# Performance work log

Measured on AMD Instinct MI355X. Metric: run time of the kernel, lower is better.

Reference implementation:

```python
import jax, jax.numpy as jnp
import numpy as np

# ---- module hyperparameters (from init_kwargs) ----
K_CURV = 1.0      # Lorentz curvature k
MAX_NORM = 1000.0 # rescale_to_max cap on space-norm (assumed)
KSIZE = 5
STRIDE = 2
PAD = 2
IN_CH = 257       # includes time dim -> 256 space channels
OUT_CH = 257
LIN_FEATS = (IN_CH - 1) * KSIZE + 1  # 1281
EPS = 1e-8


def _add_time(space):
    # time = sqrt(k + ||space||^2), concat on last axis
    time = jnp.sqrt(K_CURV + jnp.sum(space * space, axis=-1, keepdims=True))
    return jnp.concatenate([time, space], axis=-1)


def _rescale_to_max(x):
    # clamp space-norm to MAX_NORM, then recompute valid time component
    space = x[..., 1:]
    norm = jnp.sqrt(jnp.sum(space * space, axis=-1, keepdims=True))
    scale = jnp.minimum(1.0, MAX_NORM / jnp.maximum(norm, EPS))
    return _add_time(space * scale)


def setup_inputs() -> dict:
    key = jax.random.key(0)
    kx, kw, kb = jax.random.split(key, 3)
    x = jax.random.normal(kx, (16, 8192, IN_CH), dtype=jnp.float32)
    W = jax.random.normal(kw, (OUT_CH, LIN_FEATS), dtype=jnp.float32) * 0.02
    b = jax.random.normal(kb, (OUT_CH,), dtype=jnp.float32) * 0.01
    return {"x": x, "W": W, "b": b}


def reference(x, W, b):
    B, L, C = x.shape
    # pad length dim with zeros (time channel of padded frames is clamped in
    # torch, but the time channel is discarded before add_time, so only the
    # space channels matter)
    xp = jnp.pad(x, ((0, 0), (PAD, PAD), (0, 0)))
    space = xp[..., 1:]                                  # (B, Lp, C-1)
    Lp = L + 2 * PAD
    n_frames = (Lp - KSIZE) // STRIDE + 1
    # im2col gather: (n_frames, K) window indices
    idx = jnp.arange(n_frames)[:, None] * STRIDE + jnp.arange(KSIZE)[None, :]
    patches = space[:, idx, :]                           # (B, n, K, C-1)
    # torch reorders to kernel-major (k, c) layout before add_time
    ps = patches.reshape(B, n_frames, KSIZE * (C - 1))   # (B, n, K*(C-1))
    pk = _add_time(ps)                                   # (B, n, lin_feats)
    out = jnp.einsum('bnf,of->bno', pk, W) + b           # LorentzProjection
    out = _add_time(out[..., 1:])                        # manifold.projx
    out = _rescale_to_max(out)                           # rescale_after=True
    return out
```

## Files before the change

### kernel.cpp

```cpp
#include <hip/hip_runtime.h>
#include <hip/hip_bf16.h>
#include <cstdint>
#include <cstddef>

namespace {

constexpr int BATCH = 16;
constexpr int LEN   = 8192;
constexpr int CIN   = 257;
constexpr int CS    = 256;
constexpr int NF    = 4096;
constexpr int KG    = 1280;
constexpr int MT    = 128;
constexpr int NITER = 20;

constexpr size_t WT_BYTES = (size_t)CS * KG * 2;
constexpr size_t W0_OFF   = WT_BYTES;
constexpr size_t WS_NEED  = W0_OFF + (size_t)CS * 4;

typedef __attribute__((ext_vector_type(8))) short short8;
typedef __attribute__((ext_vector_type(8))) unsigned short ushort8v;
typedef __attribute__((ext_vector_type(4))) float f32x4;

__device__ __forceinline__ unsigned short f2bf_bits(float f) {
  union { __hip_bfloat16 h; unsigned short u; } cv;
  cv.h = __float2bfloat16(f);
  return cv.u;
}

__device__ __forceinline__ void async_cp16(const void* g, void* l) {
  __builtin_amdgcn_global_load_lds(
      (const __attribute__((address_space(1))) void*)g,
      (__attribute__((address_space(3))) void*)l,
      16, 0, 0);
}

}

__global__ void prep_w_kernel(const float* __restrict__ W,
                              __hip_bfloat16* __restrict__ wt,
                              float* __restrict__ w0) {
  int n = blockIdx.x;
  const float* wrow = W + (size_t)(n + 1) * 1281;
  for (int k = threadIdx.x; k < KG; k += blockDim.x)
    wt[(size_t)n * KG + k] = __float2bfloat16(wrow[1 + k]);
  if (threadIdx.x == 0) w0[n] = wrow[0];
}

__global__ __launch_bounds__(512, 2) void lorentz_fused_kernel(
    const float* __restrict__ x,
    const __hip_bfloat16* __restrict__ wt,
    const float* __restrict__ w0,
    const float* __restrict__ bvec,
    float* __restrict__ out) {
  __shared__ alignas(16) char A_lds[16384];
  __shared__ alignas(16) char B_lds[32768];
  __shared__ alignas(16) float time0_s[128];
  __shared__ alignas(16) float normsq_s[128];

  const int tid   = threadIdx.x;
  const int w     = tid >> 6;
  const int lane  = tid & 63;
  const int row16 = lane & 15;
  const int q     = lane >> 4;
  const int mh    = w >> 2;
  const int nq    = w & 3;
  const int lg    = lane >> 3;
  const int lc    = lane & 7;
  const int csw   = lc ^ lg;

  const int bx    = blockIdx.x;
  const int b     = bx >> 5;
  const int Mblk  = (bx & 31) * MT;

  const int m0 = w * 16 + lg;
  const int m1 = m0 + 8;
  const float* xb = x + (size_t)b * LEN * CIN;

  f32x4 acc[4][4];
#pragma unroll
  for (int i = 0; i < 4; ++i)
#pragma unroll
    for (int j = 0; j < 4; ++j) acc[i][j] = (f32x4){0.f, 0.f, 0.f, 0.f};

  float ssq0 = 0.f, ssq1 = 0.f;
  f32x4 a00, a01, a10, a11;

  auto loadA = [&](int it) {
    const int kk = it >> 2;
    const int c0 = (it & 3) << 6;
    const int coff = 1 + c0 + lc * 8;
    const int t0 = 2 * (Mblk + m0) + kk - 2;
    const int t1 = t0 + 16;
    a00 = (f32x4){0.f, 0.f, 0.f, 0.f};
    a01 = a00; a10 = a00; a11 = a00;
    if ((unsigned)t0 < (unsigned)LEN) {
      const float* g = xb + (size_t)t0 * CIN + coff;
      __builtin_memcpy(&a00, g, 16);
      __builtin_memcpy(&a01, g + 4, 16);
    }
    if ((unsigned)t1 < (unsigned)LEN) {
      const float* g = xb + (size_t)t1 * CIN + coff;
      __builtin_memcpy(&a10, g, 16);
      __builtin_memcpy(&a11, g + 4, 16);
    }
  };

  auto writeA = [&]() {
    ssq0 += a00[0]*a00[0] + a00[1]*a00[1] + a00[2]*a00[2] + a00[3]*a00[3]
          + a01[0]*a01[0] + a01[1]*a01[1] + a01[2]*a01[2] + a01[3]*a01[3];
    ssq1 += a10[0]*a10[0] + a10[1]*a10[1] + a10[2]*a10[2] + a10[3]*a10[3]
          + a11[0]*a11[0] + a11[1]*a11[1] + a11[2]*a11[2] + a11[3]*a11[3];
    ushort8v u0, u1;
#pragma unroll
    for (int i = 0; i < 4; ++i) {
      u0[i]     = f2bf_bits(a00[i]);
      u0[4 + i] = f2bf_bits(a01[i]);
      u1[i]     = f2bf_bits(a10[i]);
      u1[4 + i] = f2bf_bits(a11[i]);
    }
    *(ushort8v*)(A_lds + ((m0 * 8 + csw) << 4)) = u0;
    *(ushort8v*)(A_lds + ((m1 * 8 + csw) << 4)) = u1;
  };

  auto stageB = [&](int it) {
    const int k0 = it << 6;
#pragma unroll
    for (int j = 0; j < 4; ++j) {
      const int n = w * 32 + j * 8 + lg;
      async_cp16(wt + (size_t)n * KG + k0 + csw * 8, B_lds + (w * 4 + j) * 1024);
    }
  };

  auto compute = [&]() {
#pragma unroll
    for (int s = 0; s < 2; ++s) {
      const int p = (s * 4 + q) ^ lc;
      short8 bfr[4];
#pragma unroll
      for (int nt = 0; nt < 4; ++nt)
        bfr[nt] = *(const short8*)(B_lds + (((nq * 64 + nt * 16 + row16) * 8 + p) << 4));
#pragma unroll
      for (int mt = 0; mt < 4; ++mt) {
        short8 af = *(const short8*)(A_lds + (((mh * 64 + mt * 16 + row16) * 8 + p) << 4));
#pragma unroll
        for (int nt = 0; nt < 4; ++nt)
          acc[mt][nt] = __builtin_amdgcn_mfma_f32_16x16x32_bf16(
              af, bfr[nt], acc[mt][nt], 0, 0, 0);
      }
    }
  };

  loadA(0);
  for (int it = 0; it < NITER; ++it) {
    __syncthreads();
    writeA();
    stageB(it);
    if (it + 1 < NITER) loadA(it + 1);
    __syncthreads();
    compute();
  }

  __syncthreads();
  if (tid < 128) normsq_s[tid] = 0.0f;
  {
    float s0 = ssq0;
    s0 += __shfl_xor(s0, 1); s0 += __shfl_xor(s0, 2); s0 += __shfl_xor(s0, 4);
    float s1 = ssq1;
    s1 += __shfl_xor(s1, 1); s1 += __shfl_xor(s1, 2); s1 += __shfl_xor(s1, 4);
    if (lc == 0) {
      time0_s[m0] = sqrtf(1.0f + s0);
      time0_s[m1] = sqrtf(1.0f + s1);
    }
  }
  __syncthreads();

  float w0v[4], bv[4];
#pragma unroll
  for (int nt = 0; nt < 4; ++nt) {
    int n = nq * 64 + nt * 16 + row16;
    w0v[nt] = w0[n];
    bv[nt]  = bvec[1 + n];
  }

#pragma unroll
  for (int mt = 0; mt < 4; ++mt) {
    f32x4 t4 = *(const f32x4*)&time0_s[mh * 64 + mt * 16 + q * 4];
#pragma unroll
    for (int nt = 0; nt < 4; ++nt)
#pragma unroll
      for (int r = 0; r < 4; ++r)
        acc[mt][nt][r] = acc[mt][nt][r] + t4[r] * w0v[nt] + bv[nt];
#pragma unroll
    for (int r = 0; r < 4; ++r) {
      float ps = 0.f;
#pragma unroll
      for (int nt = 0; nt < 4; ++nt) ps += acc[mt][nt][r] * acc[mt][nt][r];
      ps += __shfl_xor(ps, 1);
      ps += __shfl_xor(ps, 2);
      ps += __shfl_xor(ps, 4);
      ps += __shfl_xor(ps, 8);
      if (row16 == 0) atomicAdd(&normsq_s[mh * 64 + mt * 16 + q * 4 + r], ps);
    }
  }
  __syncthreads();

#pragma unroll
  for (int mt = 0; mt < 4; ++mt) {
#pragma unroll
    for (int r = 0; r < 4; ++r) {
      int m = mh * 64 + mt * 16 + q * 4 + r;
      float nsq  = normsq_s[m];
      float norm = sqrtf(nsq);
      float scale = fminf(1.0f, 1000.0f / fmaxf(norm, 1e-8f));
      size_t ob = ((size_t)b * NF + Mblk + m) * 257;
#pragma unroll
      for (int nt = 0; nt < 4; ++nt) {
        int n = nq * 64 + nt * 16 + row16;
        out[ob + 1 + n] = acc[mt][nt][r] * scale;
      }
    }
  }
  if (tid < 128) {
    float nsq  = normsq_s[tid];
    float norm = sqrtf(nsq);
    float scale = fminf(1.0f, 1000.0f / fmaxf(norm, 1e-8f));
    size_t ob = ((size_t)b * NF + Mblk + tid) * 257;
    out[ob] = sqrtf(1.0f + scale * scale * nsq);
  }
}

__global__ void fallback_kernel(const float* __restrict__ x,
                                const float* __restrict__ W,
                                const float* __restrict__ bvec,
                                float* __restrict__ out) {
  int fid = blockIdx.x;
  int b = fid >> 12;
  int g = fid & (NF - 1);
  __shared__ float patch[1280];
  __shared__ float red[256];
  int tid = threadIdx.x;
  float ss = 0.f;
  for (int k = tid; k < 1280; k += 256) {
    int kk = k >> 8, c = k & 255;
    int t = 2 * g + kk - 2;
    float v = (t >= 0 && t < LEN) ? x[((size_t)b * LEN + t) * CIN + 1 + c] : 0.f;
    patch[k] = v;
    ss += v * v;
  }
  red[tid] = ss;
  __syncthreads();
  for (int off = 128; off > 0; off >>= 1) {
    if (tid < off) red[tid] += red[tid + off];
    __syncthreads();
  }
  float time0 = sqrtf(1.f + red[0]);
  __syncthreads();
  const float* wrow = W + (size_t)(tid + 1) * 1281;
  float acc = time0 * wrow[0] + bvec[tid + 1];
  for (int k = 0; k < 1280; ++k) acc += wrow[1 + k] * patch[k];
  red[tid] = acc * acc;
  __syncthreads();
  for (int off = 128; off > 0; off >>= 1) {
    if (tid < off) red[tid] += red[tid + off];
    __syncthreads();
  }
  float nsq = red[0];
  float norm = sqrtf(nsq);
  float scale = fminf(1.f, 1000.f / fmaxf(norm, 1e-8f));
  size_t ob = ((size_t)b * NF + g) * 257;
  out[ob + 1 + tid] = acc * scale;
  if (tid == 0) out[ob] = sqrtf(1.f + scale * scale * nsq);
}

extern "C" void kernel_launch(void* const* d_in, const int* in_sizes, int n_in,
                              void* d_out, int out_size, void* d_ws, size_t ws_size,
                              hipStream_t stream) {
  const float* x  = (const float*)d_in[0];
  const float* W  = (const float*)d_in[1];
  const float* bv = (const float*)d_in[2];
  float* out = (float*)d_out;

  if (ws_size >= WS_NEED) {
    char* ws = (char*)d_ws;
    __hip_bfloat16* wt = (__hip_bfloat16*)ws;
    float* w0          = (float*)(ws + W0_OFF);
    prep_w_kernel<<<256, 256, 0, stream>>>(W, wt, w0);
    lorentz_fused_kernel<<<BATCH * (NF / MT), 512, 0, stream>>>(x, wt, w0, bv, out);
  } else {
    fallback_kernel<<<BATCH * NF, 256, 0, stream>>>(x, W, bv, out);
  }
}
```

Before: 285.5 us.

## Drop LDS staging and feed MFMA fragments directly from global memory

```diff
diff --git a/kernel.cpp b/kernel.cpp
--- a/kernel.cpp
+++ b/kernel.cpp
@@ -19,20 +19,14 @@
 constexpr size_t WS_NEED  = W0_OFF + (size_t)CS * 4;
 
 typedef __attribute__((ext_vector_type(8))) short short8;
-typedef __attribute__((ext_vector_type(8))) unsigned short ushort8v;
 typedef __attribute__((ext_vector_type(4))) float f32x4;
+
+union bfpack { unsigned short u[8]; short8 s; };
 
 __device__ __forceinline__ unsigned short f2bf_bits(float f) {
   union { __hip_bfloat16 h; unsigned short u; } cv;
   cv.h = __float2bfloat16(f);
   return cv.u;
-}
-
-__device__ __forceinline__ void async_cp16(const void* g, void* l) {
-  __builtin_amdgcn_global_load_lds(
-      (const __attribute__((address_space(1))) void*)g,
-      (__attribute__((address_space(3))) void*)l,
-      16, 0, 0);
 }
 
 }
@@ -47,14 +41,12 @@
   if (threadIdx.x == 0) w0[n] = wrow[0];
 }
 
-__global__ __launch_bounds__(512, 2) void lorentz_fused_kernel(
+__global__ __launch_bounds__(512, 4) void lorentz_fused_kernel(
     const float* __restrict__ x,
     const __hip_bfloat16* __restrict__ wt,
     const float* __restrict__ w0,
     const float* __restrict__ bvec,
     float* __restrict__ out) {
-  __shared__ alignas(16) char A_lds[16384];
-  __shared__ alignas(16) char B_lds[32768];
   __shared__ alignas(16) float time0_s[128];
   __shared__ alignas(16) float normsq_s[128];
 
@@ -63,131 +55,113 @@
   const int lane  = tid & 63;
   const int row16 = lane & 15;
   const int q     = lane >> 4;
-  const int mh    = w >> 2;
-  const int nq    = w & 3;
-  const int lg    = lane >> 3;
-  const int lc    = lane & 7;
-  const int csw   = lc ^ lg;
+  const int wm    = w >> 1;
+  const int wn    = w & 1;
 
   const int bx    = blockIdx.x;
   const int b     = bx >> 5;
   const int Mblk  = (bx & 31) * MT;
 
-  const int m0 = w * 16 + lg;
-  const int m1 = m0 + 8;
   const float* xb = x + (size_t)b * LEN * CIN;
-
-  f32x4 acc[4][4];
-#pragma unroll
-  for (int i = 0; i < 4; ++i)
-#pragma unroll
-    for (int j = 0; j < 4; ++j) acc[i][j] = (f32x4){0.f, 0.f, 0.f, 0.f};
-
+  const int frame0 = Mblk + wm * 32 + row16;
+
+  f32x4 acc[2][8];
+#pragma unroll
+  for (int i = 0; i < 2; ++i)
+#pragma unroll
+    for (int j = 0; j < 8; ++j) acc[i][j] = (f32x4){0.f, 0.f, 0.f, 0.f};
+
+  f32x4 afA[2][4], afB[2][4];
   float ssq0 = 0.f, ssq1 = 0.f;
-  f32x4 a00, a01, a10, a11;
-
-  auto loadA = [&](int it) {
-    const int kk = it >> 2;
-    const int c0 = (it & 3) << 6;
-    const int coff = 1 + c0 + lc * 8;
-    const int t0 = 2 * (Mblk + m0) + kk - 2;
-    const int t1 = t0 + 16;
-    a00 = (f32x4){0.f, 0.f, 0.f, 0.f};
-    a01 = a00; a10 = a00; a11 = a00;
-    if ((unsigned)t0 < (unsigned)LEN) {
-      const float* g = xb + (size_t)t0 * CIN + coff;
-      __builtin_memcpy(&a00, g, 16);
-      __builtin_memcpy(&a01, g + 4, 16);
-    }
-    if ((unsigned)t1 < (unsigned)LEN) {
-      const float* g = xb + (size_t)t1 * CIN + coff;
-      __builtin_memcpy(&a10, g, 16);
-      __builtin_memcpy(&a11, g + 4, 16);
-    }
-  };
-
-  auto writeA = [&]() {
-    ssq0 += a00[0]*a00[0] + a00[1]*a00[1] + a00[2]*a00[2] + a00[3]*a00[3]
-          + a01[0]*a01[0] + a01[1]*a01[1] + a01[2]*a01[2] + a01[3]*a01[3];
-    ssq1 += a10[0]*a10[0] + a10[1]*a10[1] + a10[2]*a10[2] + a10[3]*a10[3]
-          + a11[0]*a11[0] + a11[1]*a11[1] + a11[2]*a11[2] + a11[3]*a11[3];
-    ushort8v u0, u1;
+
+  auto loadA = [&](int it, f32x4 (&af)[2][4]) {
+#pragma unroll
+    for (int mt = 0; mt < 2; ++mt) {
+      const int t = 2 * (frame0 + mt * 16) + (it >> 2) - 2;
+      af[mt][0] = (f32x4){0.f, 0.f, 0.f, 0.f};
+      af[mt][1] = af[mt][0];
+      af[mt][2] = af[mt][0];
+      af[mt][3] = af[mt][0];
+      if ((unsigned)t < (unsigned)LEN) {
+        const float* g = xb + (size_t)t * CIN + 1 + ((it & 3) << 6) + q * 8;
+        __builtin_memcpy(&af[mt][0], g, 16);
+        __builtin_memcpy(&af[mt][1], g + 4, 16);
+        __builtin_memcpy(&af[mt][2], g + 32, 16);
+        __builtin_memcpy(&af[mt][3], g + 36, 16);
+      }
+    }
+  };
+
+  auto cvt2 = [&](const f32x4& lo, const f32x4& hi) -> short8 {
+    bfpack p;
 #pragma unroll
     for (int i = 0; i < 4; ++i) {
-      u0[i]     = f2bf_bits(a00[i]);
-      u0[4 + i] = f2bf_bits(a01[i]);
-      u1[i]     = f2bf_bits(a10[i]);
-      u1[4 + i] = f2bf_bits(a11[i]);
-    }
-    *(ushort8v*)(A_lds + ((m0 * 8 + csw) << 4)) = u0;
-    *(ushort8v*)(A_lds + ((m1 * 8 + csw) << 4)) = u1;
-  };
-
-  auto stageB = [&](int it) {
-    const int k0 = it << 6;
-#pragma unroll
-    for (int j = 0; j < 4; ++j) {
-      const int n = w * 32 + j * 8 + lg;
-      async_cp16(wt + (size_t)n * KG + k0 + csw * 8, B_lds + (w * 4 + j) * 1024);
-    }
-  };
-
-  auto compute = [&]() {
-#pragma unroll
-    for (int s = 0; s < 2; ++s) {
-      const int p = (s * 4 + q) ^ lc;
-      short8 bfr[4];
-#pragma unroll
-      for (int nt = 0; nt < 4; ++nt)
-        bfr[nt] = *(const short8*)(B_lds + (((nq * 64 + nt * 16 + row16) * 8 + p) << 4));
-#pragma unroll
-      for (int mt = 0; mt < 4; ++mt) {
-        short8 af = *(const short8*)(A_lds + (((mh * 64 + mt * 16 + row16) * 8 + p) << 4));
-#pragma unroll
-        for (int nt = 0; nt < 4; ++nt)
-          acc[mt][nt] = __builtin_amdgcn_mfma_f32_16x16x32_bf16(
-              af, bfr[nt], acc[mt][nt], 0, 0, 0);
+      p.u[i]     = f2bf_bits(lo[i]);
+      p.u[4 + i] = f2bf_bits(hi[i]);
+    }
+    return p.s;
+  };
+
+  auto mfma_half = [&](int it, int s, f32x4 (&cur)[2][4]) {
+    const int ko = (it << 6) + s * 32 + q * 8;
+    short8 bb[8];
+#pragma unroll
+    for (int nt = 0; nt < 8; ++nt) {
+      const int n = wn * 128 + nt * 16 + row16;
+      bb[nt] = *(const short8*)(wt + (size_t)n * KG + ko);
+    }
+    short8 ab0 = cvt2(cur[0][s * 2], cur[0][s * 2 + 1]);
+    short8 ab1 = cvt2(cur[1][s * 2], cur[1][s * 2 + 1]);
+    if (wn == 0) {
+#pragma unroll
+      for (int i = 0; i < 4; ++i) {
+        ssq0 += cur[0][s*2][i] * cur[0][s*2][i] + cur[0][s*2+1][i] * cur[0][s*2+1][i];
+        ssq1 += cur[1][s*2][i] * cur[1][s*2][i] + cur[1][s*2+1][i] * cur[1][s*2+1][i];
       }
     }
-  };
-
-  loadA(0);
-  for (int it = 0; it < NITER; ++it) {
-    __syncthreads();
-    writeA();
-    stageB(it);
-    if (it + 1 < NITER) loadA(it + 1);
-    __syncthreads();
-    compute();
-  }
-
-  __syncthreads();
+#pragma unroll
+    for (int nt = 0; nt < 8; ++nt) {
+      acc[0][nt] = __builtin_amdgcn_mfma_f32_16x16x32_bf16(ab0, bb[nt], acc[0][nt], 0, 0, 0);
+      acc[1][nt] = __builtin_amdgcn_mfma_f32_16x16x32_bf16(ab1, bb[nt], acc[1][nt], 0, 0, 0);
+    }
+  };
+
+  auto body = [&](int it, f32x4 (&cur)[2][4], f32x4 (&nxt)[2][4]) {
+    if (it + 1 < NITER) loadA(it + 1, nxt);
+    mfma_half(it, 0, cur);
+    mfma_half(it, 1, cur);
+  };
+
+  loadA(0, afA);
+  for (int it = 0; it < NITER; it += 2) {
+    body(it,     afA, afB);
+    body(it + 1, afB, afA);
+  }
+
   if (tid < 128) normsq_s[tid] = 0.0f;
   {
-    float s0 = ssq0;
-    s0 += __shfl_xor(s0, 1); s0 += __shfl_xor(s0, 2); s0 += __shfl_xor(s0, 4);
-    float s1 = ssq1;
-    s1 += __shfl_xor(s1, 1); s1 += __shfl_xor(s1, 2); s1 += __shfl_xor(s1, 4);
-    if (lc == 0) {
-      time0_s[m0] = sqrtf(1.0f + s0);
-      time0_s[m1] = sqrtf(1.0f + s1);
-    }
-  }
-  __syncthreads();
-
-  float w0v[4], bv[4];
-#pragma unroll
-  for (int nt = 0; nt < 4; ++nt) {
-    int n = nq * 64 + nt * 16 + row16;
+    float s0 = ssq0; s0 += __shfl_xor(s0, 16); s0 += __shfl_xor(s0, 32);
+    float s1 = ssq1; s1 += __shfl_xor(s1, 16); s1 += __shfl_xor(s1, 32);
+    if (wn == 0 && q == 0) {
+      time0_s[wm * 32 + row16]      = sqrtf(1.0f + s0);
+      time0_s[wm * 32 + 16 + row16] = sqrtf(1.0f + s1);
+    }
+  }
+  __syncthreads();
+
+  float w0v[8], bv[8];
+#pragma unroll
+  for (int nt = 0; nt < 8; ++nt) {
+    int n = wn * 128 + nt * 16 + row16;
     w0v[nt] = w0[n];
     bv[nt]  = bvec[1 + n];
   }
 
 #pragma unroll
-  for (int mt = 0; mt < 4; ++mt) {
-    f32x4 t4 = *(const f32x4*)&time0_s[mh * 64 + mt * 16 + q * 4];
-#pragma unroll
-    for (int nt = 0; nt < 4; ++nt)
+  for (int mt = 0; mt < 2; ++mt) {
+    f32x4 t4 = *(const f32x4*)&time0_s[wm * 32 + mt * 16 + q * 4];
+#pragma unroll
+    for (int nt = 0; nt < 8; ++nt)
 #pragma unroll
       for (int r = 0; r < 4; ++r)
         acc[mt][nt][r] = acc[mt][nt][r] + t4[r] * w0v[nt] + bv[nt];
@@ -195,30 +169,28 @@
     for (int r = 0; r < 4; ++r) {
       float ps = 0.f;
 #pragma unroll
-      for (int nt = 0; nt < 4; ++nt) ps += acc[mt][nt][r] * acc[mt][nt][r];
+      for (int nt = 0; nt < 8; ++nt) ps += acc[mt][nt][r] * acc[mt][nt][r];
       ps += __shfl_xor(ps, 1);
       ps += __shfl_xor(ps, 2);
       ps += __shfl_xor(ps, 4);
       ps += __shfl_xor(ps, 8);
-      if (row16 == 0) atomicAdd(&normsq_s[mh * 64 + mt * 16 + q * 4 + r], ps);
-    }
-  }
-  __syncthreads();
-
-#pragma unroll
-  for (int mt = 0; mt < 4; ++mt) {
+      if (row16 == 0) atomicAdd(&normsq_s[wm * 32 + mt * 16 + q * 4 + r], ps);
+    }
+  }
+  __syncthreads();
+
+#pragma unroll
+  for (int mt = 0; mt < 2; ++mt) {
 #pragma unroll
     for (int r = 0; r < 4; ++r) {
-      int m = mh * 64 + mt * 16 + q * 4 + r;
+      int m = wm * 32 + mt * 16 + q * 4 + r;
       float nsq  = normsq_s[m];
       float norm = sqrtf(nsq);
       float scale = fminf(1.0f, 1000.0f / fmaxf(norm, 1e-8f));
       size_t ob = ((size_t)b * NF + Mblk + m) * 257;
 #pragma unroll
-      for (int nt = 0; nt < 4; ++nt) {
-        int n = nq * 64 + nt * 16 + row16;
-        out[ob + 1 + n] = acc[mt][nt][r] * scale;
-      }
+      for (int nt = 0; nt < 8; ++nt)
+        out[ob + 1 + wn * 128 + nt * 16 + row16] = acc[mt][nt][r] * scale;
     }
   }
   if (tid < 128) {
```

Result: slower. 1.044 ms (+265.6%).
